# Kernel tuning notes

Measured on AMD Instinct MI355X. Metric: run time of the kernel, lower is better.

The kernel has to match this reference:

```python
import jax, jax.numpy as jnp
import numpy as np

D_MODEL, N_HEADS, D_STATE, N_GROUPS, CHUNK = 2048, 32, 64, 1, 256
BATCH, SEQLEN = 2, 4096


def setup_inputs() -> dict:
    key = jax.random.key(0)
    ks = jax.random.split(key, 8)
    s = 0.02
    d, h, n, g = D_MODEL, N_HEADS, D_STATE, N_GROUPS
    return {
        "x": jax.random.normal(ks[0], (BATCH, SEQLEN, d), jnp.float32),
        "A_log": jnp.log(jnp.arange(1, h + 1, dtype=jnp.float32)),
        "D": jnp.ones((h,), jnp.float32),
        "B_w": jax.random.normal(ks[1], (g * n, d), jnp.float32) * s,
        "B_b": jnp.zeros((g * n,), jnp.float32),
        "C_w": jax.random.normal(ks[2], (g * n, d), jnp.float32) * s,
        "C_b": jnp.zeros((g * n,), jnp.float32),
        "dt_w": jax.random.normal(ks[3], (h, d), jnp.float32) * s,
        "dt_b": jnp.zeros((h,), jnp.float32),
        "out_w": jax.random.normal(ks[4], (d, d), jnp.float32) * s,
        "out_b": jnp.zeros((d,), jnp.float32),
    }


def segsum(v):
    # v: [..., T] -> [..., T, T]; out[i,j] = sum_{k=j+1..i} v[k] for i>=j, -inf else
    cs = jnp.cumsum(v, axis=-1)
    seg = cs[..., :, None] - cs[..., None, :]
    T = v.shape[-1]
    mask = jnp.tril(jnp.ones((T, T), bool))
    return jnp.where(mask, seg, -jnp.inf)


def _ssd(x, A_log, D, B_w, B_b, C_w, C_b, dt_w, dt_b, out_w, out_b):
    b, t, d = x.shape
    h = A_log.shape[0]
    n = B_w.shape[0] // N_GROUPS
    p = d // h
    l = CHUNK
    c = t // l

    A = -jnp.exp(A_log.astype(jnp.float32))                      # [h]
    B = (x @ B_w.T + B_b).reshape(b, t, N_GROUPS, n)             # g=1
    C = (x @ C_w.T + C_b).reshape(b, t, N_GROUPS, n)
    B = jnp.broadcast_to(B, (b, t, h, n))                        # repeat groups -> heads
    C = jnp.broadcast_to(C, (b, t, h, n))
    dt = jax.nn.softplus(x @ dt_w.T + dt_b)                      # [b,t,h]
    xh = x.reshape(b, t, h, p)

    # chunked SSD (Mamba2 mamba_chunk_scan_combined math)
    xc = xh.reshape(b, c, l, h, p)
    Bc = B.reshape(b, c, l, h, n)
    Cc = C.reshape(b, c, l, h, n)
    dtc = dt.reshape(b, c, l, h)
    dA = jnp.transpose(dtc * A, (0, 3, 1, 2))                    # [b,h,c,l]
    A_cumsum = jnp.cumsum(dA, axis=-1)                           # [b,h,c,l]

    # 1. intra-chunk (diagonal blocks)
    L = jnp.exp(segsum(dA))                                      # [b,h,c,l,l]
    xdt = xc * dtc[..., None]                                    # [b,c,l,h,p]
    Y_diag = jnp.einsum('bclhn,bcshn,bhcls,bcshp->bclhp', Cc, Bc, L, xdt)

    # 2. per-chunk final states
    decay_states = jnp.exp(A_cumsum[..., -1:] - A_cumsum)        # [b,h,c,l]
    states = jnp.einsum('bclhn,bhcl,bclhp->bchpn', Bc, decay_states, xdt)

    # 3. inter-chunk recurrence on chunk states
    states = jnp.concatenate([jnp.zeros_like(states[:, :1]), states], axis=1)  # [b,c+1,h,p,n]
    dA_last = jnp.pad(A_cumsum[..., -1], ((0, 0), (0, 0), (1, 0)))             # [b,h,c+1]
    decay_chunk = jnp.exp(segsum(dA_last))                                     # [b,h,c+1,c+1]
    new_states = jnp.einsum('bhzc,bchpn->bzhpn', decay_chunk, states)
    prev_states = new_states[:, :-1]                                           # [b,c,h,p,n]

    # 4. state -> output contribution
    state_decay_out = jnp.exp(A_cumsum)                          # [b,h,c,l]
    Y_off = jnp.einsum('bclhn,bchpn,bhcl->bclhp', Cc, prev_states, state_decay_out)

    Y = (Y_diag + Y_off).reshape(b, t, h, p) + D[None, None, :, None] * xh
    return Y.reshape(b, t, d) @ out_w.T + out_b


def reference(x, A_log, D, B_w, B_b, C_w, C_b, dt_w, dt_b, out_w, out_b):
    return _ssd(x, A_log, D, B_w, B_b, C_w, C_b, dt_w, dt_b, out_w, out_b)
```

## Files before the change

kernel.cpp:

```cpp
#include <hip/hip_runtime.h>
#include <hip/hip_bf16.h>
#include <math.h>

namespace {
constexpr int kDModel = 2048;
constexpr int kHeads  = 32;
constexpr int kState  = 64;
constexpr int kP      = 64;
constexpr int kChunk  = 256;
constexpr int kNChunk = 16;
constexpr int kBatch  = 2;
constexpr int kSeq    = 4096;
constexpr int kM      = kBatch * kSeq;
}

typedef __bf16 bf16_t;
typedef __attribute__((ext_vector_type(8))) __bf16 bf16x8;
typedef __attribute__((ext_vector_type(4))) __bf16 bf16x4;
typedef __attribute__((ext_vector_type(4))) float f32x4;
typedef __attribute__((ext_vector_type(16))) float f32x16;

__device__ __forceinline__ void gload_lds16(const void* g, void* l) {
    __builtin_amdgcn_global_load_lds(
        (const __attribute__((address_space(1))) void*)g,
        (__attribute__((address_space(3))) void*)l,
        16, 0, 0);
}

__global__ __launch_bounds__(256)
void gemm_bcdt(const bf16_t* __restrict__ A, const bf16_t* __restrict__ W,
               const float* __restrict__ b0, const float* __restrict__ b1,
               const float* __restrict__ b2,
               bf16_t* __restrict__ o0h, bf16_t* __restrict__ o1h,
               float* __restrict__ o2f)
{
    constexpr int K = kDModel;
    __shared__ __bf16 AstS[64 * 32];
    __shared__ __bf16 WstS[128 * 32];
    const int tid  = threadIdx.x;
    const int lane = tid & 63;
    const int wave = tid >> 6;
    const int wm = (wave >> 1) * 32;
    const int wn = (wave & 1) * 64;
    const int l15 = lane & 15, quad = lane >> 4;
    const int m0 = blockIdx.y * 64;
    const int n0 = blockIdx.x * 128;
    const int u0 = tid, u1 = tid + 256;

    f32x4 acc[2][4];
    #pragma unroll
    for (int i = 0; i < 2; ++i)
        #pragma unroll
        for (int j = 0; j < 4; ++j)
            acc[i][j] = (f32x4){0.f, 0.f, 0.f, 0.f};

    for (int k0 = 0; k0 < K; k0 += 32) {
        gload_lds16(A + (size_t)(m0 + (tid >> 2)) * K + k0 + (tid & 3) * 8, AstS + tid * 8);
        gload_lds16(W + (size_t)(n0 + (u0 >> 2)) * K + k0 + (u0 & 3) * 8, WstS + u0 * 8);
        gload_lds16(W + (size_t)(n0 + (u1 >> 2)) * K + k0 + (u1 & 3) * 8, WstS + u1 * 8);
        __syncthreads();
        bf16x8 af[2], bfr[4];
        #pragma unroll
        for (int mi = 0; mi < 2; ++mi)
            af[mi] = *reinterpret_cast<const bf16x8*>(&AstS[(wm + mi * 16 + l15) * 32 + quad * 8]);
        #pragma unroll
        for (int ni = 0; ni < 4; ++ni)
            bfr[ni] = *reinterpret_cast<const bf16x8*>(&WstS[(wn + ni * 16 + l15) * 32 + quad * 8]);
        #pragma unroll
        for (int mi = 0; mi < 2; ++mi)
            #pragma unroll
            for (int ni = 0; ni < 4; ++ni)
                acc[mi][ni] = __builtin_amdgcn_mfma_f32_16x16x32_bf16(
                    af[mi], bfr[ni], acc[mi][ni], 0, 0, 0);
        __syncthreads();
    }

    #pragma unroll
    for (int mi = 0; mi < 2; ++mi) {
        #pragma unroll
        for (int reg = 0; reg < 4; ++reg) {
            const int r = m0 + wm + mi * 16 + quad * 4 + reg;
            #pragma unroll
            for (int ni = 0; ni < 4; ++ni) {
                const float v = acc[mi][ni][reg];
                const int n = n0 + wn + ni * 16 + l15;
                if (n < 64) {
                    o0h[(size_t)r * 64 + n] = (bf16_t)(v + b0[n]);
                } else if (n < 128) {
                    o1h[(size_t)r * 64 + (n - 64)] = (bf16_t)(v + b1[n - 64]);
                } else if (n < 160) {
                    float z = v + b2[n - 128];
                    o2f[(size_t)r * 32 + (n - 128)] = (z > 20.f) ? z : log1pf(expf(z));
                }
            }
        }
    }
}

__global__ __launch_bounds__(512, 2)
void gemm256_out(const bf16_t* __restrict__ Ap, const bf16_t* __restrict__ Bp,
                 const float* __restrict__ bias, float* __restrict__ C)
{
    constexpr int M = 8192, N = 2048, NT = 2048 / 32;
    __shared__ __bf16 Ab[3][4 * 256 * 8];
    __shared__ __bf16 Bb[3][4 * 256 * 8];
    const int tid  = threadIdx.x;
    const int lane = tid & 63;
    const int wave = tid >> 6;
    const int row32 = lane & 31, half = lane >> 5;
    const int bid = blockIdx.x;
    const int mt = (bid & 7) * 4 + ((bid >> 3) & 3);
    const int nt = bid >> 5;
    const int m0 = mt * 256;
    const int n0 = nt * 256;
    const int wm = (wave >> 2) * 128;
    const int wn = (wave & 3) * 64;

    const int u0 = tid, u1 = tid + 512;
    auto stage = [&](int t2, int stb) {
        const int ks0 = t2 * 4;
        const bf16_t* As = Ap + ((size_t)ks0 * M + m0) * 8;
        const bf16_t* Bs = Bp + ((size_t)ks0 * N + n0) * 8;
        __bf16* Al = &Ab[stb][0];
        __bf16* Bl = &Bb[stb][0];
        gload_lds16(As + ((size_t)(u0 >> 8) * M + (u0 & 255)) * 8, Al + u0 * 8);
        gload_lds16(As + ((size_t)(u1 >> 8) * M + (u1 & 255)) * 8, Al + u1 * 8);
        gload_lds16(Bs + ((size_t)(u0 >> 8) * N + (u0 & 255)) * 8, Bl + u0 * 8);
        gload_lds16(Bs + ((size_t)(u1 >> 8) * N + (u1 & 255)) * 8, Bl + u1 * 8);
    };

    f32x16 acc[4][2];
    #pragma unroll
    for (int i = 0; i < 4; ++i)
        #pragma unroll
        for (int j = 0; j < 2; ++j)
            #pragma unroll
            for (int e = 0; e < 16; ++e)
                acc[i][j][e] = 0.f;

    stage(0, 0);
    stage(1, 1);
    asm volatile("s_waitcnt vmcnt(4)" ::: "memory");
    __builtin_amdgcn_s_barrier();

    int cur = 0;
    for (int t = 0; t < NT; ++t) {
        const __bf16* Ac = &Ab[cur][0];
        const __bf16* Bc = &Bb[cur][0];
        int stb = cur + 2; if (stb >= 3) stb -= 3;

        bf16x8 af[4], bfr[2];
        #pragma unroll
        for (int mf = 0; mf < 4; ++mf)
            af[mf] = *reinterpret_cast<const bf16x8*>(
                &Ac[(half * 256 + wm + mf * 32 + row32) * 8]);
        #pragma unroll
        for (int nf = 0; nf < 2; ++nf)
            bfr[nf] = *reinterpret_cast<const bf16x8*>(
                &Bc[(half * 256 + wn + nf * 32 + row32) * 8]);
        if (t < NT - 2) stage(t + 2, stb);
        __builtin_amdgcn_s_setprio(1);
        #pragma unroll
        for (int mf = 0; mf < 4; ++mf)
            #pragma unroll
            for (int nf = 0; nf < 2; ++nf)
                acc[mf][nf] = __builtin_amdgcn_mfma_f32_32x32x16_bf16(
                    af[mf], bfr[nf], acc[mf][nf], 0, 0, 0);
        __builtin_amdgcn_s_setprio(0);

        #pragma unroll
        for (int mf = 0; mf < 4; ++mf)
            af[mf] = *reinterpret_cast<const bf16x8*>(
                &Ac[((2 + half) * 256 + wm + mf * 32 + row32) * 8]);
        #pragma unroll
        for (int nf = 0; nf < 2; ++nf)
            bfr[nf] = *reinterpret_cast<const bf16x8*>(
                &Bc[((2 + half) * 256 + wn + nf * 32 + row32) * 8]);
        __builtin_amdgcn_s_setprio(1);
        #pragma unroll
        for (int mf = 0; mf < 4; ++mf)
            #pragma unroll
            for (int nf = 0; nf < 2; ++nf)
                acc[mf][nf] = __builtin_amdgcn_mfma_f32_32x32x16_bf16(
                    af[mf], bfr[nf], acc[mf][nf], 0, 0, 0);
        __builtin_amdgcn_s_setprio(0);

        if (t < NT - 2) {
            asm volatile("s_waitcnt vmcnt(4)" ::: "memory");
        } else if (t < NT - 1) {
            asm volatile("s_waitcnt vmcnt(0)" ::: "memory");
        }
        if (t < NT - 1) __builtin_amdgcn_s_barrier();
        cur = cur + 1; if (cur == 3) cur = 0;
    }

    float bia[2];
    #pragma unroll
    for (int nf = 0; nf < 2; ++nf) bia[nf] = bias[n0 + wn + nf * 32 + row32];
    #pragma unroll
    for (int mf = 0; mf < 4; ++mf) {
        #pragma unroll
        for (int nf = 0; nf < 2; ++nf) {
            #pragma unroll
            for (int reg = 0; reg < 16; ++reg) {
                const int r = m0 + wm + mf * 32 + (reg & 3) + 8 * (reg >> 2) + 4 * half;
                const int c = n0 + wn + nf * 32 + row32;
                C[(size_t)r * N + c] = acc[mf][nf][reg] + bia[nf];
            }
        }
    }
}

__global__ __launch_bounds__(256)
void cvt_bf16_kernel(const float* __restrict__ src, bf16_t* __restrict__ dst, int n)
{
    const int i = (blockIdx.x * 256 + threadIdx.x) * 4;
    if (i + 3 < n) {
        const float4 v = *reinterpret_cast<const float4*>(src + i);
        dst[i + 0] = (bf16_t)v.x;
        dst[i + 1] = (bf16_t)v.y;
        dst[i + 2] = (bf16_t)v.z;
        dst[i + 3] = (bf16_t)v.w;
    }
}

__global__ __launch_bounds__(256)
void pack_wob_kernel(const float* __restrict__ W, bf16_t* __restrict__ Wp)
{
    const int idx = blockIdx.x * 256 + threadIdx.x;
    const int n = idx >> 8, ks = idx & 255;
    const float4 v0 = *reinterpret_cast<const float4*>(W + (size_t)n * 2048 + ks * 8);
    const float4 v1 = *reinterpret_cast<const float4*>(W + (size_t)n * 2048 + ks * 8 + 4);
    bf16x8 o;
    o[0] = (__bf16)v0.x; o[1] = (__bf16)v0.y; o[2] = (__bf16)v0.z; o[3] = (__bf16)v0.w;
    o[4] = (__bf16)v1.x; o[5] = (__bf16)v1.y; o[6] = (__bf16)v1.z; o[7] = (__bf16)v1.w;
    *reinterpret_cast<bf16x8*>(Wp + ((size_t)ks * 2048 + n) * 8) = o;
}

__global__ __launch_bounds__(256)
void pack_w_kernel(const float* __restrict__ B_w, const float* __restrict__ C_w,
                   const float* __restrict__ dt_w, bf16_t* __restrict__ wcat)
{
    const int idx = blockIdx.x * 256 + threadIdx.x;
    const int r = idx >> 11, k = idx & 2047;
    float v = 0.f;
    if (r < 64)       v = B_w[r * 2048 + k];
    else if (r < 128) v = C_w[(r - 64) * 2048 + k];
    else if (r < 160) v = dt_w[(r - 128) * 2048 + k];
    wcat[idx] = (bf16_t)v;
}

__global__ __launch_bounds__(kChunk)
void dtcumsum_kernel(const float* __restrict__ dtm, const float* __restrict__ A_log,
                     float* __restrict__ Acs)
{
    const int blk = blockIdx.x;
    const int ci = blk & (kNChunk - 1);
    const int hi = (blk >> 4) & (kHeads - 1);
    const int bi = blk >> 9;
    const int t = threadIdx.x;
    const float Ah = -expf(A_log[hi]);
    __shared__ float s[kChunk];
    s[t] = dtm[((size_t)bi * kSeq + ci * kChunk + t) * kHeads + hi] * Ah;
    __syncthreads();
    for (int off = 1; off < kChunk; off <<= 1) {
        const float add = (t >= off) ? s[t - off] : 0.f;
        __syncthreads();
        s[t] += add;
        __syncthreads();
    }
    Acs[((size_t)(bi * kHeads + hi) * kNChunk + ci) * kChunk + t] = s[t];
}

__global__ __launch_bounds__(256)
void bT_kernel(const bf16_t* __restrict__ Bb16, bf16_t* __restrict__ bTg)
{
    const int ci = blockIdx.x & (kNChunk - 1);
    const int bi = blockIdx.x >> 4;
    const size_t rowbase = (size_t)bi * kSeq + ci * kChunk;
    __shared__ __bf16 T[64 * 264];
    const int tid = threadIdx.x;
    bf16x8 v[8];
    #pragma unroll
    for (int e = 0; e < 8; ++e)
        v[e] = *reinterpret_cast<const bf16x8*>(Bb16 + (rowbase + tid) * 64 + e * 8);
    #pragma unroll
    for (int e = 0; e < 8; ++e)
        #pragma unroll
        for (int j = 0; j < 8; ++j)
            T[(e * 8 + j) * 264 + tid] = v[e][j];
    __syncthreads();
    const int n = tid >> 2, seg = (tid & 3) * 64;
    bf16_t* dst = bTg + ((size_t)(bi * kNChunk + ci)) * (64 * 256) + n * 256 + seg;
    #pragma unroll
    for (int j = 0; j < 8; ++j) {
        *reinterpret_cast<bf16x8*>(dst + j * 8) =
            *reinterpret_cast<const bf16x8*>(&T[n * 264 + seg + j * 8]);
    }
}

__global__ __launch_bounds__(256)
void xdtT_kernel(const bf16_t* __restrict__ xb, const float* __restrict__ dtm,
                 bf16_t* __restrict__ xdtT)
{
    const int blk = blockIdx.x;
    const int hi = blk & (kHeads - 1);
    const int ci = (blk >> 5) & (kNChunk - 1);
    const int bi = blk >> 9;
    const size_t rowbase = (size_t)bi * kSeq + ci * kChunk;
    __shared__ __bf16 T[64 * 264];
    const int tid = threadIdx.x;
    const float d = dtm[(rowbase + tid) * kHeads + hi];
    bf16x8 v[8];
    #pragma unroll
    for (int e = 0; e < 8; ++e)
        v[e] = *reinterpret_cast<const bf16x8*>(xb + (rowbase + tid) * kDModel + hi * kP + e * 8);
    #pragma unroll
    for (int e = 0; e < 8; ++e)
        #pragma unroll
        for (int j = 0; j < 8; ++j)
            T[(e * 8 + j) * 264 + tid] = (__bf16)((float)v[e][j] * d);
    __syncthreads();
    const int p = tid >> 2, seg = (tid & 3) * 64;
    bf16_t* dst = xdtT + (size_t)blk * (64 * 256) + p * 256 + seg;
    #pragma unroll
    for (int j = 0; j < 8; ++j) {
        *reinterpret_cast<bf16x8*>(dst + j * 8) =
            *reinterpret_cast<const bf16x8*>(&T[p * 264 + seg + j * 8]);
    }
}

__global__ __launch_bounds__(256)
void states_mfma(const bf16_t* __restrict__ xdtT, const bf16_t* __restrict__ bTg,
                 const float* __restrict__ Acs, float* __restrict__ states)
{
    const int blk = blockIdx.x;
    const int hi = blk & (kHeads - 1);
    const int ci = (blk >> 5) & (kNChunk - 1);
    const int bi = blk >> 9;
    __shared__ __bf16 Xa[64 * 264];
    __shared__ __bf16 Bt[64 * 264];
    __shared__ float dec[kChunk];
    const int tid = threadIdx.x;
    const int lane = tid & 63;
    const int wave = tid >> 6;
    const int l15 = lane & 15, quad = lane >> 4;

    const float* acs = Acs + ((size_t)(bi * kHeads + hi) * kNChunk + ci) * kChunk;
    dec[tid] = expf(acs[kChunk - 1] - acs[tid]);
    __syncthreads();

    const bf16_t* bsrc = bTg + ((size_t)(bi * kNChunk + ci)) * (64 * 256);
    const bf16_t* xsrc = xdtT + (size_t)blk * (64 * 256);
    #pragma unroll
    for (int e = 0; e < 8; ++e) {
        const int u = e * 256 + tid;
        const int r = u >> 5, seg = (u & 31) * 8;
        *reinterpret_cast<bf16x8*>(&Bt[r * 264 + seg]) =
            *reinterpret_cast<const bf16x8*>(bsrc + r * 256 + seg);
        bf16x8 xv = *reinterpret_cast<const bf16x8*>(xsrc + r * 256 + seg);
        bf16x8 xo;
        #pragma unroll
        for (int j = 0; j < 8; ++j)
            xo[j] = (__bf16)((float)xv[j] * dec[seg + j]);
        *reinterpret_cast<bf16x8*>(&Xa[r * 264 + seg]) = xo;
    }
    __syncthreads();

    f32x4 acc[4];
    #pragma unroll
    for (int ni = 0; ni < 4; ++ni) acc[ni] = (f32x4){0.f, 0.f, 0.f, 0.f};
    #pragma unroll
    for (int kk = 0; kk < 8; ++kk) {
        const bf16x8 af = *reinterpret_cast<const bf16x8*>(
            &Xa[(wave * 16 + l15) * 264 + kk * 32 + quad * 8]);
        #pragma unroll
        for (int ni = 0; ni < 4; ++ni) {
            const bf16x8 bf = *reinterpret_cast<const bf16x8*>(
                &Bt[(ni * 16 + l15) * 264 + kk * 32 + quad * 8]);
            acc[ni] = __builtin_amdgcn_mfma_f32_16x16x32_bf16(af, bf, acc[ni], 0, 0, 0);
        }
    }
    float* sp = states + (size_t)blk * (kP * kState);
    #pragma unroll
    for (int reg = 0; reg < 4; ++reg) {
        const int p = wave * 16 + quad * 4 + reg;
        #pragma unroll
        for (int ni = 0; ni < 4; ++ni)
            sp[(size_t)p * kState + ni * 16 + l15] = acc[ni][reg];
    }
}

__global__ __launch_bounds__(256)
void chunkscan_kernel(const float* __restrict__ states, const float* __restrict__ Acs,
                      bf16_t* __restrict__ prevsb)
{
    const int q  = blockIdx.x & 15;
    const int hi = (blockIdx.x >> 4) & (kHeads - 1);
    const int bi = blockIdx.x >> 9;
    const int e  = q * 256 + threadIdx.x;
    __shared__ float ea[kNChunk];
    if (threadIdx.x < kNChunk)
        ea[threadIdx.x] = expf(Acs[((size_t)(bi * kHeads + hi) * kNChunk + threadIdx.x)
                                   * kChunk + kChunk - 1]);
    __syncthreads();
    float P = 0.f;
    prevsb[((size_t)(bi * kNChunk + 0) * kHeads + hi) * (kP * kState) + e] = (bf16_t)0.f;
    for (int c = 1; c < kNChunk; ++c) {
        P = fmaf(ea[c - 1], P,
                 states[((size_t)(bi * kNChunk + (c - 1)) * kHeads + hi) * (kP * kState) + e]);
        prevsb[((size_t)(bi * kNChunk + c) * kHeads + hi) * (kP * kState) + e] = (bf16_t)P;
    }
}

__global__ __launch_bounds__(256)
void ychunk_mfma(const bf16_t* __restrict__ Bb16, const bf16_t* __restrict__ Cb16,
                 const bf16_t* __restrict__ xdtT, const float* __restrict__ Acs,
                 const bf16_t* __restrict__ prevsb, const float* __restrict__ dtm,
                 const float* __restrict__ Dvec, bf16_t* __restrict__ Yp)
{
    const int blk = blockIdx.x;
    const int hi = blk & (kHeads - 1);
    const int ci = (blk >> 5) & (kNChunk - 1);
    const int bi = blk >> 9;
    __shared__ float acs_s[kChunk];
    __shared__ float dts[kChunk];
    __shared__ __bf16 Cs[256 * 72];
    __shared__ __bf16 Ps[64 * 72];
    __shared__ __bf16 Bs[64 * 72];
    __shared__ __bf16 Xt[64 * 72];
    __shared__ __bf16 Sp[64 * 72];
    const int tid = threadIdx.x;
    const int lane = tid & 63;
    const int wave = tid >> 6;
    const int l15 = lane & 15, quad = lane >> 4;
    const int mrow = wave * 16 + quad * 4;
    const size_t rowbase = (size_t)bi * kSeq + ci * kChunk;
    const bf16_t* xdsrc = xdtT + (size_t)blk * (64 * 256);

    acs_s[tid] = Acs[((size_t)(bi * kHeads + hi) * kNChunk + ci) * kChunk + tid];
    dts[tid]   = dtm[(rowbase + tid) * kHeads + hi];
    #pragma unroll
    for (int e = 0; e < 8; ++e) {
        const int u = e * 256 + tid;
        const int r = u >> 3, seg = (u & 7) * 8;
        *reinterpret_cast<bf16x8*>(&Cs[r * 72 + seg]) =
            *reinterpret_cast<const bf16x8*>(Cb16 + (rowbase + r) * 64 + seg);
    }
    const bf16_t* pp = prevsb + ((size_t)(bi * kNChunk + ci) * kHeads + hi) * (kP * kState);
    #pragma unroll
    for (int e = 0; e < 2; ++e) {
        const int u = e * 256 + tid;
        const int r = u >> 3, seg = (u & 7) * 8;
        *reinterpret_cast<bf16x8*>(&Ps[r * 72 + seg]) =
            *reinterpret_cast<const bf16x8*>(pp + r * 64 + seg);
    }
    __syncthreads();

    f32x4 yacc[4][4];
    #pragma unroll
    for (int lt = 0; lt < 4; ++lt) {
        #pragma unroll
        for (int ni = 0; ni < 4; ++ni) yacc[lt][ni] = (f32x4){0.f, 0.f, 0.f, 0.f};
        const bf16x8 af0 = *reinterpret_cast<const bf16x8*>(
            &Cs[(lt * 64 + wave * 16 + l15) * 72 + quad * 8]);
        const bf16x8 af1 = *reinterpret_cast<const bf16x8*>(
            &Cs[(lt * 64 + wave * 16 + l15) * 72 + 32 + quad * 8]);
        #pragma unroll
        for (int ni = 0; ni < 4; ++ni) {
            const bf16x8 b0 = *reinterpret_cast<const bf16x8*>(&Ps[(ni * 16 + l15) * 72 + quad * 8]);
            const bf16x8 b1 = *reinterpret_cast<const bf16x8*>(&Ps[(ni * 16 + l15) * 72 + 32 + quad * 8]);
            yacc[lt][ni] = __builtin_amdgcn_mfma_f32_16x16x32_bf16(af0, b0, yacc[lt][ni], 0, 0, 0);
            yacc[lt][ni] = __builtin_amdgcn_mfma_f32_16x16x32_bf16(af1, b1, yacc[lt][ni], 0, 0, 0);
        }
        float es[4];
        #pragma unroll
        for (int reg = 0; reg < 4; ++reg) es[reg] = expf(acs_s[lt * 64 + mrow + reg]);
        #pragma unroll
        for (int ni = 0; ni < 4; ++ni)
            #pragma unroll
            for (int reg = 0; reg < 4; ++reg) yacc[lt][ni][reg] *= es[reg];
    }

    const float Dh = Dvec[hi];
    for (int st = 0; st < 4; ++st) {
        __syncthreads();
        #pragma unroll
        for (int e = 0; e < 2; ++e) {
            const int u = e * 256 + tid;
            const int r = u >> 3, seg = (u & 7) * 8;
            *reinterpret_cast<bf16x8*>(&Bs[r * 72 + seg]) =
                *reinterpret_cast<const bf16x8*>(Bb16 + (rowbase + st * 64 + r) * 64 + seg);
            *reinterpret_cast<bf16x8*>(&Xt[r * 72 + seg]) =
                *reinterpret_cast<const bf16x8*>(xdsrc + r * 256 + st * 64 + seg);
        }
        __syncthreads();
        #pragma unroll
        for (int lt = 0; lt < 4; ++lt) {
            if (lt < st) continue;
            const bf16x8 af0 = *reinterpret_cast<const bf16x8*>(
                &Cs[(lt * 64 + wave * 16 + l15) * 72 + quad * 8]);
            const bf16x8 af1 = *reinterpret_cast<const bf16x8*>(
                &Cs[(lt * 64 + wave * 16 + l15) * 72 + 32 + quad * 8]);
            f32x4 sacc[4];
            #pragma unroll
            for (int ni = 0; ni < 4; ++ni) sacc[ni] = (f32x4){0.f, 0.f, 0.f, 0.f};
            #pragma unroll
            for (int ni = 0; ni < 4; ++ni) {
                const bf16x8 b0 = *reinterpret_cast<const bf16x8*>(&Bs[(ni * 16 + l15) * 72 + quad * 8]);
                const bf16x8 b1 = *reinterpret_cast<const bf16x8*>(&Bs[(ni * 16 + l15) * 72 + 32 + quad * 8]);
                sacc[ni] = __builtin_amdgcn_mfma_f32_16x16x32_bf16(af0, b0, sacc[ni], 0, 0, 0);
                sacc[ni] = __builtin_amdgcn_mfma_f32_16x16x32_bf16(af1, b1, sacc[ni], 0, 0, 0);
            }
            #pragma unroll
            for (int reg = 0; reg < 4; ++reg) {
                const int l = lt * 64 + mrow + reg;
                const float al = acs_s[l];
                #pragma unroll
                for (int ni = 0; ni < 4; ++ni) {
                    const int scol = ni * 16 + l15;
                    const int sg = st * 64 + scol;
                    float v = sacc[ni][reg] * expf(al - acs_s[sg]);
                    if (st == lt && sg > l) v = 0.f;
                    Sp[(mrow + reg) * 72 + scol] = (__bf16)v;
                }
            }
            __syncthreads();
            const bf16x8 as0 = *reinterpret_cast<const bf16x8*>(&Sp[(wave * 16 + l15) * 72 + quad * 8]);
            const bf16x8 as1 = *reinterpret_cast<const bf16x8*>(&Sp[(wave * 16 + l15) * 72 + 32 + quad * 8]);
            #pragma unroll
            for (int ni = 0; ni < 4; ++ni) {
                const bf16x8 x0 = *reinterpret_cast<const bf16x8*>(&Xt[(ni * 16 + l15) * 72 + quad * 8]);
                const bf16x8 x1 = *reinterpret_cast<const bf16x8*>(&Xt[(ni * 16 + l15) * 72 + 32 + quad * 8]);
                yacc[lt][ni] = __builtin_amdgcn_mfma_f32_16x16x32_bf16(as0, x0, yacc[lt][ni], 0, 0, 0);
                yacc[lt][ni] = __builtin_amdgcn_mfma_f32_16x16x32_bf16(as1, x1, yacc[lt][ni], 0, 0, 0);
            }
            if (lt == st) {
                #pragma unroll
                for (int reg = 0; reg < 4; ++reg) {
                    const int lrow = mrow + reg;
                    const size_t tg = rowbase + lt * 64 + lrow;
                    const float dinv = 1.f / dts[lt * 64 + lrow];
                    #pragma unroll
                    for (int ni = 0; ni < 4; ++ni) {
                        const int p = ni * 16 + l15;
                        const float xv = (float)Xt[p * 72 + lrow] * dinv;
                        const float v = yacc[lt][ni][reg] + Dh * xv;
                        Yp[((size_t)(hi * 8 + (p >> 3)) * (size_t)kM + tg) * 8 + (p & 7)] = (bf16_t)v;
                    }
                }
            }
            __syncthreads();
        }
    }
}

extern "C" void kernel_launch(void* const* d_in, const int* in_sizes, int n_in,
                              void* d_out, int out_size, void* d_ws, size_t ws_size,
                              hipStream_t stream)
{
    (void)in_sizes; (void)n_in; (void)out_size; (void)ws_size;
    const float* x     = (const float*)d_in[0];
    const float* A_log = (const float*)d_in[1];
    const float* Dvec  = (const float*)d_in[2];
    const float* B_w   = (const float*)d_in[3];
    const float* B_b   = (const float*)d_in[4];
    const float* C_w   = (const float*)d_in[5];
    const float* C_b   = (const float*)d_in[6];
    const float* dt_w  = (const float*)d_in[7];
    const float* dt_b  = (const float*)d_in[8];
    const float* out_w = (const float*)d_in[9];
    const float* out_b = (const float*)d_in[10];
    float* out = (float*)d_out;

    float* ws = (float*)d_ws;
    float* dtm    = ws;
    float* Acs    = dtm + (size_t)kM * kHeads;
    float* states = Acs + (size_t)kBatch * kHeads * kNChunk * kChunk;
    bf16_t* prevsb = (bf16_t*)(states + (size_t)kBatch * kNChunk * kHeads * kP * kState);
    bf16_t* xb    = prevsb + (size_t)kBatch * kNChunk * kHeads * kP * kState;
    bf16_t* Y     = xb;
    bf16_t* Bb16  = xb + (size_t)kM * kDModel;
    bf16_t* Cb16  = Bb16 + (size_t)kM * kState;
    bf16_t* xdtT  = Cb16 + (size_t)kM * kState;
    bf16_t* bTg   = xdtT + (size_t)kM * kDModel;
    bf16_t* wcat  = bTg + (size_t)kBatch * kNChunk * kState * kChunk;
    bf16_t* wob   = wcat + (size_t)256 * kDModel;

    const dim3 blk(256);
    cvt_bf16_kernel<<<dim3(kM * kDModel / 1024), blk, 0, stream>>>(x, xb, kM * kDModel);
    pack_wob_kernel<<<dim3(kDModel * 256 / 256), blk, 0, stream>>>(out_w, wob);
    pack_w_kernel<<<dim3(256 * kDModel / 256), blk, 0, stream>>>(B_w, C_w, dt_w, wcat);
    gemm_bcdt<<<dim3(2, kM / 64), blk, 0, stream>>>(xb, wcat, B_b, C_b, dt_b,
                                                    Bb16, Cb16, dtm);
    dtcumsum_kernel<<<dim3(kBatch * kHeads * kNChunk), dim3(kChunk), 0, stream>>>(dtm, A_log, Acs);
    bT_kernel<<<dim3(kBatch * kNChunk), blk, 0, stream>>>(Bb16, bTg);
    xdtT_kernel<<<dim3(kBatch * kNChunk * kHeads), blk, 0, stream>>>(xb, dtm, xdtT);
    states_mfma<<<dim3(kBatch * kNChunk * kHeads), blk, 0, stream>>>(xdtT, bTg, Acs, states);
    chunkscan_kernel<<<dim3(kBatch * kHeads * 16), blk, 0, stream>>>(states, Acs, prevsb);
    ychunk_mfma<<<dim3(kBatch * kNChunk * kHeads), blk, 0, stream>>>(
        Bb16, Cb16, xdtT, Acs, prevsb, dtm, Dvec, Y);
    gemm256_out<<<dim3(256), dim3(512), 0, stream>>>(Y, wob, out_b, out);
}
```

Before: 383.5 us.

## Split ychunk kernel across 64-row query tiles for more parallel blocks

The ychunk kernel now launches one block per (batch, chunk, head, 64-row tile) instead of one block per chunk-head, giving four times as many blocks. Each block handles one row tile against its causal prefix of key tiles, with smaller shared memory and fewer accumulator registers. This raises occupancy and spreads the triangular work over more CUs. In exchange, B, xdt and the prev-state tiles are reloaded redundantly by several blocks, and the work per block is uneven (tile lt runs lt+1 iterations).

```diff
diff --git a/kernel.cpp b/kernel.cpp
--- a/kernel.cpp
+++ b/kernel.cpp
@@ -420,13 +420,13 @@
                  const float* __restrict__ Dvec, bf16_t* __restrict__ Yp)
 {
     const int blk = blockIdx.x;
-    const int hi = blk & (kHeads - 1);
-    const int ci = (blk >> 5) & (kNChunk - 1);
-    const int bi = blk >> 9;
+    const int lt = blk & 3;
+    const int hi = (blk >> 2) & (kHeads - 1);
+    const int ci = (blk >> 7) & (kNChunk - 1);
+    const int bi = blk >> 11;
     __shared__ float acs_s[kChunk];
-    __shared__ float dts[kChunk];
-    __shared__ __bf16 Cs[256 * 72];
-    __shared__ __bf16 Ps[64 * 72];
+    __shared__ float dts_s[64];
+    __shared__ __bf16 Cs[64 * 72];
     __shared__ __bf16 Bs[64 * 72];
     __shared__ __bf16 Xt[64 * 72];
     __shared__ __bf16 Sp[64 * 72];
@@ -436,54 +436,47 @@
     const int l15 = lane & 15, quad = lane >> 4;
     const int mrow = wave * 16 + quad * 4;
     const size_t rowbase = (size_t)bi * kSeq + ci * kChunk;
-    const bf16_t* xdsrc = xdtT + (size_t)blk * (64 * 256);
+    const bf16_t* xdsrc = xdtT + ((size_t)((bi * kNChunk + ci) * kHeads + hi)) * (64 * 256);
 
     acs_s[tid] = Acs[((size_t)(bi * kHeads + hi) * kNChunk + ci) * kChunk + tid];
-    dts[tid]   = dtm[(rowbase + tid) * kHeads + hi];
-    #pragma unroll
-    for (int e = 0; e < 8; ++e) {
+    if (tid < 64) dts_s[tid] = dtm[(rowbase + lt * 64 + tid) * kHeads + hi];
+    const bf16_t* pp = prevsb + ((size_t)(bi * kNChunk + ci) * kHeads + hi) * (kP * kState);
+    #pragma unroll
+    for (int e = 0; e < 2; ++e) {
         const int u = e * 256 + tid;
         const int r = u >> 3, seg = (u & 7) * 8;
         *reinterpret_cast<bf16x8*>(&Cs[r * 72 + seg]) =
-            *reinterpret_cast<const bf16x8*>(Cb16 + (rowbase + r) * 64 + seg);
-    }
-    const bf16_t* pp = prevsb + ((size_t)(bi * kNChunk + ci) * kHeads + hi) * (kP * kState);
-    #pragma unroll
-    for (int e = 0; e < 2; ++e) {
-        const int u = e * 256 + tid;
-        const int r = u >> 3, seg = (u & 7) * 8;
-        *reinterpret_cast<bf16x8*>(&Ps[r * 72 + seg]) =
+            *reinterpret_cast<const bf16x8*>(Cb16 + (rowbase + lt * 64 + r) * 64 + seg);
+        *reinterpret_cast<bf16x8*>(&Bs[r * 72 + seg]) =
             *reinterpret_cast<const bf16x8*>(pp + r * 64 + seg);
     }
     __syncthreads();
 
-    f32x4 yacc[4][4];
-    #pragma unroll
-    for (int lt = 0; lt < 4; ++lt) {
-        #pragma unroll
-        for (int ni = 0; ni < 4; ++ni) yacc[lt][ni] = (f32x4){0.f, 0.f, 0.f, 0.f};
-        const bf16x8 af0 = *reinterpret_cast<const bf16x8*>(
-            &Cs[(lt * 64 + wave * 16 + l15) * 72 + quad * 8]);
-        const bf16x8 af1 = *reinterpret_cast<const bf16x8*>(
-            &Cs[(lt * 64 + wave * 16 + l15) * 72 + 32 + quad * 8]);
-        #pragma unroll
-        for (int ni = 0; ni < 4; ++ni) {
-            const bf16x8 b0 = *reinterpret_cast<const bf16x8*>(&Ps[(ni * 16 + l15) * 72 + quad * 8]);
-            const bf16x8 b1 = *reinterpret_cast<const bf16x8*>(&Ps[(ni * 16 + l15) * 72 + 32 + quad * 8]);
-            yacc[lt][ni] = __builtin_amdgcn_mfma_f32_16x16x32_bf16(af0, b0, yacc[lt][ni], 0, 0, 0);
-            yacc[lt][ni] = __builtin_amdgcn_mfma_f32_16x16x32_bf16(af1, b1, yacc[lt][ni], 0, 0, 0);
-        }
+    bf16x8 af[2];
+    af[0] = *reinterpret_cast<const bf16x8*>(&Cs[(wave * 16 + l15) * 72 + quad * 8]);
+    af[1] = *reinterpret_cast<const bf16x8*>(&Cs[(wave * 16 + l15) * 72 + 32 + quad * 8]);
+
+    f32x4 yacc[4];
+    #pragma unroll
+    for (int ni = 0; ni < 4; ++ni) yacc[ni] = (f32x4){0.f, 0.f, 0.f, 0.f};
+    #pragma unroll
+    for (int ni = 0; ni < 4; ++ni) {
+        const bf16x8 b0 = *reinterpret_cast<const bf16x8*>(&Bs[(ni * 16 + l15) * 72 + quad * 8]);
+        const bf16x8 b1 = *reinterpret_cast<const bf16x8*>(&Bs[(ni * 16 + l15) * 72 + 32 + quad * 8]);
+        yacc[ni] = __builtin_amdgcn_mfma_f32_16x16x32_bf16(af[0], b0, yacc[ni], 0, 0, 0);
+        yacc[ni] = __builtin_amdgcn_mfma_f32_16x16x32_bf16(af[1], b1, yacc[ni], 0, 0, 0);
+    }
+    {
         float es[4];
         #pragma unroll
         for (int reg = 0; reg < 4; ++reg) es[reg] = expf(acs_s[lt * 64 + mrow + reg]);
         #pragma unroll
         for (int ni = 0; ni < 4; ++ni)
             #pragma unroll
-            for (int reg = 0; reg < 4; ++reg) yacc[lt][ni][reg] *= es[reg];
-    }
-
-    const float Dh = Dvec[hi];
-    for (int st = 0; st < 4; ++st) {
+            for (int reg = 0; reg < 4; ++reg) yacc[ni][reg] *= es[reg];
+    }
+
+    for (int st = 0; st <= lt; ++st) {
         __syncthreads();
         #pragma unroll
         for (int e = 0; e < 2; ++e) {
@@ -495,62 +488,53 @@
                 *reinterpret_cast<const bf16x8*>(xdsrc + r * 256 + st * 64 + seg);
         }
         __syncthreads();
-        #pragma unroll
-        for (int lt = 0; lt < 4; ++lt) {
-            if (lt < st) continue;
-            const bf16x8 af0 = *reinterpret_cast<const bf16x8*>(
-                &Cs[(lt * 64 + wave * 16 + l15) * 72 + quad * 8]);
-            const bf16x8 af1 = *reinterpret_cast<const bf16x8*>(
-                &Cs[(lt * 64 + wave * 16 + l15) * 72 + 32 + quad * 8]);
-            f32x4 sacc[4];
-            #pragma unroll
-            for (int ni = 0; ni < 4; ++ni) sacc[ni] = (f32x4){0.f, 0.f, 0.f, 0.f};
+        f32x4 sacc[4];
+        #pragma unroll
+        for (int ni = 0; ni < 4; ++ni) sacc[ni] = (f32x4){0.f, 0.f, 0.f, 0.f};
+        #pragma unroll
+        for (int ni = 0; ni < 4; ++ni) {
+            const bf16x8 b0 = *reinterpret_cast<const bf16x8*>(&Bs[(ni * 16 + l15) * 72 + quad * 8]);
+            const bf16x8 b1 = *reinterpret_cast<const bf16x8*>(&Bs[(ni * 16 + l15) * 72 + 32 + quad * 8]);
+            sacc[ni] = __builtin_amdgcn_mfma_f32_16x16x32_bf16(af[0], b0, sacc[ni], 0, 0, 0);
+            sacc[ni] = __builtin_amdgcn_mfma_f32_16x16x32_bf16(af[1], b1, sacc[ni], 0, 0, 0);
+        }
+        #pragma unroll
+        for (int reg = 0; reg < 4; ++reg) {
+            const int l = lt * 64 + mrow + reg;
+            const float al = acs_s[l];
             #pragma unroll
             for (int ni = 0; ni < 4; ++ni) {
-                const bf16x8 b0 = *reinterpret_cast<const bf16x8*>(&Bs[(ni * 16 + l15) * 72 + quad * 8]);
-                const bf16x8 b1 = *reinterpret_cast<const bf16x8*>(&Bs[(ni * 16 + l15) * 72 + 32 + quad * 8]);
-                sacc[ni] = __builtin_amdgcn_mfma_f32_16x16x32_bf16(af0, b0, sacc[ni], 0, 0, 0);
-                sacc[ni] = __builtin_amdgcn_mfma_f32_16x16x32_bf16(af1, b1, sacc[ni], 0, 0, 0);
+                const int scol = ni * 16 + l15;
+                const int sg = st * 64 + scol;
+                float v = sacc[ni][reg] * expf(al - acs_s[sg]);
+                if (st == lt && sg > l) v = 0.f;
+                Sp[(mrow + reg) * 72 + scol] = (__bf16)v;
             }
-            #pragma unroll
-            for (int reg = 0; reg < 4; ++reg) {
-                const int l = lt * 64 + mrow + reg;
-                const float al = acs_s[l];
-                #pragma unroll
-                for (int ni = 0; ni < 4; ++ni) {
-                    const int scol = ni * 16 + l15;
-                    const int sg = st * 64 + scol;
-                    float v = sacc[ni][reg] * expf(al - acs_s[sg]);
-                    if (st == lt && sg > l) v = 0.f;
-                    Sp[(mrow + reg) * 72 + scol] = (__bf16)v;
-                }
-            }
-            __syncthreads();
-            const bf16x8 as0 = *reinterpret_cast<const bf16x8*>(&Sp[(wave * 16 + l15) * 72 + quad * 8]);
-            const bf16x8 as1 = *reinterpret_cast<const bf16x8*>(&Sp[(wave * 16 + l15) * 72 + 32 + quad * 8]);
-            #pragma unroll
-            for (int ni = 0; ni < 4; ++ni) {
-                const bf16x8 x0 = *reinterpret_cast<const bf16x8*>(&Xt[(ni * 16 + l15) * 72 + quad * 8]);
-                const bf16x8 x1 = *reinterpret_cast<const bf16x8*>(&Xt[(ni * 16 + l15) * 72 + 32 + quad * 8]);
-                yacc[lt][ni] = __builtin_amdgcn_mfma_f32_16x16x32_bf16(as0, x0, yacc[lt][ni], 0, 0, 0);
-                yacc[lt][ni] = __builtin_amdgcn_mfma_f32_16x16x32_bf16(as1, x1, yacc[lt][ni], 0, 0, 0);
-            }
-            if (lt == st) {
-                #pragma unroll
-                for (int reg = 0; reg < 4; ++reg) {
-                    const int lrow = mrow + reg;
-                    const size_t tg = rowbase + lt * 64 + lrow;
-                    const float dinv = 1.f / dts[lt * 64 + lrow];
-                    #pragma unroll
-                    for (int ni = 0; ni < 4; ++ni) {
-                        const int p = ni * 16 + l15;
-                        const float xv = (float)Xt[p * 72 + lrow] * dinv;
-                        const float v = yacc[lt][ni][reg] + Dh * xv;
-                        Yp[((size_t)(hi * 8 + (p >> 3)) * (size_t)kM + tg) * 8 + (p & 7)] = (bf16_t)v;
-                    }
-                }
-            }
-            __syncthreads();
+        }
+        __syncthreads();
+        const bf16x8 as0 = *reinterpret_cast<const bf16x8*>(&Sp[(wave * 16 + l15) * 72 + quad * 8]);
+        const bf16x8 as1 = *reinterpret_cast<const bf16x8*>(&Sp[(wave * 16 + l15) * 72 + 32 + quad * 8]);
+        #pragma unroll
+        for (int ni = 0; ni < 4; ++ni) {
+            const bf16x8 x0 = *reinterpret_cast<const bf16x8*>(&Xt[(ni * 16 + l15) * 72 + quad * 8]);
+            const bf16x8 x1 = *reinterpret_cast<const bf16x8*>(&Xt[(ni * 16 + l15) * 72 + 32 + quad * 8]);
+            yacc[ni] = __builtin_amdgcn_mfma_f32_16x16x32_bf16(as0, x0, yacc[ni], 0, 0, 0);
+            yacc[ni] = __builtin_amdgcn_mfma_f32_16x16x32_bf16(as1, x1, yacc[ni], 0, 0, 0);
+        }
+    }
+
+    const float Dh = Dvec[hi];
+    #pragma unroll
+    for (int reg = 0; reg < 4; ++reg) {
+        const int lrow = mrow + reg;
+        const size_t tg = rowbase + lt * 64 + lrow;
+        const float dinv = 1.f / dts_s[lrow];
+        #pragma unroll
+        for (int ni = 0; ni < 4; ++ni) {
+            const int p = ni * 16 + l15;
+            const float xv = (float)Xt[p * 72 + lrow] * dinv;
+            const float v = yacc[ni][reg] + Dh * xv;
+            Yp[((size_t)(hi * 8 + (p >> 3)) * (size_t)kM + tg) * 8 + (p & 7)] = (bf16_t)v;
         }
     }
 }
@@ -598,7 +582,7 @@
     xdtT_kernel<<<dim3(kBatch * kNChunk * kHeads), blk, 0, stream>>>(xb, dtm, xdtT);
     states_mfma<<<dim3(kBatch * kNChunk * kHeads), blk, 0, stream>>>(xdtT, bTg, Acs, states);
     chunkscan_kernel<<<dim3(kBatch * kHeads * 16), blk, 0, stream>>>(states, Acs, prevsb);
-    ychunk_mfma<<<dim3(kBatch * kNChunk * kHeads), blk, 0, stream>>>(
+    ychunk_mfma<<<dim3(kBatch * kNChunk * kHeads * 4), blk, 0, stream>>>(
         Bb16, Cb16, xdtT, Acs, prevsb, dtm, Dvec, Y);
     gemm256_out<<<dim3(256), dim3(512), 0, stream>>>(Y, wob, out_b, out);
 }
```

After: 364.7 us. 1.05x faster.
